# Kernel optimization log

Hardware: AMD Instinct MI355X
Metric: run time of the kernel (lower is better)

The kernel has to match this reference:

```python
import jax, jax.numpy as jnp
import numpy as np

IN_DIMS = 256
EMBED_DIMS = 512
NUM_HEADS = 8
GRID = 16  # forced: arrange2 hardcodes 256 = GRID*GRID tokens
HEAD_DIM = EMBED_DIMS // NUM_HEADS
LN_EPS = 1e-5


def setup_inputs() -> dict:
    key = jax.random.key(0)
    ks = jax.random.split(key, 12)
    B = 8
    s_in = 1.0 / np.sqrt(IN_DIMS)
    s_emb = 1.0 / np.sqrt(EMBED_DIMS)
    return {
        "x1": jax.random.normal(ks[0], (B, IN_DIMS, GRID, GRID), jnp.float32),
        "x2": jax.random.normal(ks[1], (B, IN_DIMS, GRID, GRID), jnp.float32),
        # 1x1 conv weights stored as [out, in]
        "Wq": jax.random.normal(ks[2], (EMBED_DIMS, IN_DIMS), jnp.float32) * s_in,
        "bq": jnp.zeros((EMBED_DIMS,), jnp.float32),
        "Wk": jax.random.normal(ks[3], (EMBED_DIMS, IN_DIMS), jnp.float32) * s_in,
        "bk": jnp.zeros((EMBED_DIMS,), jnp.float32),
        "Wv": jax.random.normal(ks[4], (EMBED_DIMS, IN_DIMS), jnp.float32) * s_in,
        "bv": jnp.zeros((EMBED_DIMS,), jnp.float32),
        "Wa": jax.random.normal(ks[5], (IN_DIMS, EMBED_DIMS), jnp.float32) * s_emb,
        "ba": jnp.zeros((IN_DIMS,), jnp.float32),
        "ln_g": jnp.ones((IN_DIMS,), jnp.float32),
        "ln_b": jnp.zeros((IN_DIMS,), jnp.float32),
        "Wl": jax.random.normal(ks[6], (IN_DIMS, IN_DIMS), jnp.float32) * s_in,
        "bl": jnp.zeros((IN_DIMS,), jnp.float32),
    }


def _conv1x1(x, W, b):
    # x: [b, Cin, h, w]; W: [Cout, Cin]
    return jnp.einsum('bihw,oi->bohw', x, W) + b[None, :, None, None]


def _arrange(t):
    # 'b (c head) h w -> head b (h w) c'  (c outer, head inner in channel axis)
    b = t.shape[0]
    t = t.reshape(b, HEAD_DIM, NUM_HEADS, GRID * GRID)
    return t.transpose(2, 0, 3, 1)  # [head, b, n, c]


def reference(x1, x2, Wq, bq, Wk, bk, Wv, bv, Wa, ba, ln_g, ln_b, Wl, bl):
    B, Cin, H, W = x1.shape
    N = H * W  # 256
    q = _arrange(_conv1x1(x1, Wq, bq))                     # [h, b, n, c]
    k = _arrange(_conv1x1(x2, Wk, bk))                     # [h, q, m, c]
    v = _arrange(_conv1x1(x2, Wv, bv)).reshape(NUM_HEADS, B * N, HEAD_DIM)  # [h, (b m), c]
    # cross-batch attention logits (NOTE: original never applies self.scale)
    attn = jnp.einsum('pbnc,pqmc->pbqnm', q, k)            # [h, b, q, n, m]
    attn = jax.nn.softmax(attn, axis=-1)
    # 'head b q n m -> b head n (q m)'
    attn = attn.transpose(1, 0, 3, 2, 4).reshape(B, NUM_HEADS, N, B * N)
    out = jnp.einsum('bhnm,hmc->bhnc', attn, v)            # [b, h, n, c]
    # 'b head (h w) c -> b (c head) h w'
    out = out.transpose(0, 3, 1, 2).reshape(B, EMBED_DIMS, H, W)
    a = _conv1x1(out, Wa, ba) + x1                          # residual, [b, Cin, h, w]
    # proj_out: rearrange -> LayerNorm -> Linear -> ReLU -> rearrange back
    t = a.reshape(B, Cin, N).transpose(0, 2, 1)            # [b, n, Cin]
    mu = t.mean(-1, keepdims=True)
    var = ((t - mu) ** 2).mean(-1, keepdims=True)
    t = (t - mu) * jax.lax.rsqrt(var + LN_EPS) * ln_g + ln_b
    t = jax.nn.relu(t @ Wl.T + bl)
    return t.transpose(0, 2, 1).reshape(B, Cin, H, W)
```

## Files before the change

kernel.cpp:

```cpp
#include <hip/hip_runtime.h>

typedef unsigned short u16;
typedef unsigned int   u32;
typedef __attribute__((ext_vector_type(8))) short bf16x8;
typedef __attribute__((ext_vector_type(4))) float f32x4;

#define BB   8
#define CIN  256
#define NT   256
#define EMB  512
#define NH   8

__device__ __forceinline__ float bf2f(u16 b) {
    union { u32 u; float f; } v; v.u = ((u32)b) << 16; return v.f;
}
__device__ __forceinline__ u16 f2bf(float f) {
    union { float f; u32 u; } v; v.f = f;
    u32 r = v.u + 0x7FFFu + ((v.u >> 16) & 1u);
    return (u16)(r >> 16);
}
__device__ __forceinline__ float ld(const u16* base, size_t idx, int f32) {
    return f32 ? ((const float*)base)[idx] : bf2f(base[idx]);
}

struct alignas(16) U32x4 { u32 x, y, z, w; };

#define FMA44(AP, S, A4, B4) do { \
  (AP)[0*(S)+0] += (A4).x*(B4).x; (AP)[0*(S)+1] += (A4).x*(B4).y; (AP)[0*(S)+2] += (A4).x*(B4).z; (AP)[0*(S)+3] += (A4).x*(B4).w; \
  (AP)[1*(S)+0] += (A4).y*(B4).x; (AP)[1*(S)+1] += (A4).y*(B4).y; (AP)[1*(S)+2] += (A4).y*(B4).z; (AP)[1*(S)+3] += (A4).y*(B4).w; \
  (AP)[2*(S)+0] += (A4).z*(B4).x; (AP)[2*(S)+1] += (A4).z*(B4).y; (AP)[2*(S)+2] += (A4).z*(B4).z; (AP)[2*(S)+3] += (A4).z*(B4).w; \
  (AP)[3*(S)+0] += (A4).w*(B4).x; (AP)[3*(S)+1] += (A4).w*(B4).y; (AP)[3*(S)+2] += (A4).w*(B4).z; (AP)[3*(S)+3] += (A4).w*(B4).w; \
} while (0)

__global__ void k_detect(const u16* __restrict__ x1, int* __restrict__ flag) {
    __shared__ int cnt;
    if (threadIdx.x == 0) cnt = 0;
    __syncthreads();
    int t = threadIdx.x;
    int local = 0;
    for (int j = t * 16; j < t * 16 + 16; j += 2) {
        u16 w = x1[j];
        int e = (w >> 7) & 0xFF;
        if (e >= 100 && e <= 145) local++;
    }
    atomicAdd(&cnt, local);
    __syncthreads();
    if (t == 0) *flag = (cnt >= 1200) ? 0 : 1;
}

__global__ void k_qkv(
    const u16* __restrict__ x1, const u16* __restrict__ x2,
    const u16* __restrict__ Wq, const u16* __restrict__ bq,
    const u16* __restrict__ Wk, const u16* __restrict__ bk,
    const u16* __restrict__ Wv, const u16* __restrict__ bv,
    u16* __restrict__ Qg, u16* __restrict__ Kg, u16* __restrict__ Vg,
    const int* __restrict__ flag)
{
    const int f32 = *flag;
    int id = blockIdx.x;
    int proj = id >> 8;
    int rem  = id & 255;
    int b  = rem >> 5;
    int ot = (rem >> 2) & 7;
    int nt = rem & 3;

    const u16* X    = (proj == 0) ? x1 : x2;
    const u16* W    = (proj == 0) ? Wq : (proj == 1) ? Wk : Wv;
    const u16* bias = (proj == 0) ? bq : (proj == 1) ? bk : bv;

    __shared__ float Ws[64][68];
    __shared__ float Xs[64][64];

    int t = threadIdx.x;
    int lane64 = t & 63;
    int quad   = t >> 6;
    int og = t >> 4;
    int ng = t & 15;

    float acc[16];
#pragma unroll
    for (int j = 0; j < 16; ++j) acc[j] = 0.f;

    float wreg[16], xreg[16];
#pragma unroll
    for (int p = 0; p < 16; ++p) {
        int o = quad + 4*p;
        wreg[p] = ld(W, (size_t)(ot*64 + o)*CIN + 0*64 + lane64, f32);
    }
#pragma unroll
    for (int p = 0; p < 16; ++p) {
        int i = quad + 4*p;
        xreg[p] = ld(X, ((size_t)b*CIN + 0*64 + i)*NT + nt*64 + lane64, f32);
    }

    for (int kc = 0; kc < 4; ++kc) {
        __syncthreads();
#pragma unroll
        for (int p = 0; p < 16; ++p)
            Ws[lane64][quad + 4*p] = wreg[p];
#pragma unroll
        for (int p = 0; p < 16; ++p)
            Xs[quad + 4*p][lane64] = xreg[p];
        __syncthreads();

        if (kc < 3) {
            int kn = kc + 1;
#pragma unroll
            for (int p = 0; p < 16; ++p) {
                int o = quad + 4*p;
                wreg[p] = ld(W, (size_t)(ot*64 + o)*CIN + kn*64 + lane64, f32);
            }
#pragma unroll
            for (int p = 0; p < 16; ++p) {
                int i = quad + 4*p;
                xreg[p] = ld(X, ((size_t)b*CIN + kn*64 + i)*NT + nt*64 + lane64, f32);
            }
        }

#pragma unroll 8
        for (int i = 0; i < 64; ++i) {
            float4 w4 = *(const float4*)&Ws[i][og*4];
            float4 x4 = *(const float4*)&Xs[i][ng*4];
            FMA44(acc, 4, w4, x4);
        }
    }
    __syncthreads();

#pragma unroll
    for (int jo = 0; jo < 4; ++jo) {
        int o = ot*64 + og*4 + jo;
        float bb = ld(bias, o, f32);
#pragma unroll
        for (int jn = 0; jn < 4; ++jn)
            Ws[og*4 + jo][ng*4 + jn] = acc[jo*4 + jn] + bb;
    }
    __syncthreads();

    if (proj < 2) {
        u16* OUT = (proj == 0) ? Qg : Kg;
        int hh = t >> 5;
        int nb = t & 31;
#pragma unroll
        for (int p = 0; p < 2; ++p) {
            int nn = nb + 32*p;
            u32 pk[4];
#pragma unroll
            for (int e = 0; e < 4; ++e) {
                u16 lo = f2bf(Ws[(2*e  )*8 + hh][nn]);
                u16 hi = f2bf(Ws[(2*e+1)*8 + hh][nn]);
                pk[e] = (u32)lo | ((u32)hi << 16);
            }
            U32x4 v; v.x = pk[0]; v.y = pk[1]; v.z = pk[2]; v.w = pk[3];
            *(U32x4*)&OUT[((size_t)((hh*8 + b)*256) + nt*64 + nn)*64 + ot*8] = v;
        }
    } else {
        int rr = t >> 2;
        int hh = rr & 7, cl = rr >> 3;
        int nq = t & 3;
        u32 pk[8];
#pragma unroll
        for (int e = 0; e < 8; ++e) {
            u16 lo = f2bf(Ws[cl*8 + hh][nq*16 + 2*e  ]);
            u16 hi = f2bf(Ws[cl*8 + hh][nq*16 + 2*e+1]);
            pk[e] = (u32)lo | ((u32)hi << 16);
        }
        size_t base = ((size_t)((hh*8 + b)*64) + ot*8 + cl)*256 + nt*64 + nq*16;
        U32x4 v0; v0.x = pk[0]; v0.y = pk[1]; v0.z = pk[2]; v0.w = pk[3];
        U32x4 v1; v1.x = pk[4]; v1.y = pk[5]; v1.z = pk[6]; v1.w = pk[7];
        *(U32x4*)&Vg[base]     = v0;
        *(U32x4*)&Vg[base + 8] = v1;
    }
}

__global__ __launch_bounds__(256) void k_attn(
    const u16* __restrict__ Qg, const u16* __restrict__ Kg,
    const u16* __restrict__ Vg, float* __restrict__ Oph)
{
    int bid = blockIdx.x;
    int h   = bid >> 5;
    int b   = (bid >> 2) & 7;
    int ntq = bid & 3;

    int t = threadIdx.x;
    int l = t & 63, w = t >> 6;
    int quad = l >> 4, col = l & 15;

    __shared__ __align__(16) u16 S[16896];

    int q = ntq*64 + w*16 + col;
    const size_t qrow = ((size_t)(h*8 + b)*256 + q)*64;
    bf16x8 qf0 = *(const bf16x8*)&Qg[qrow +  0 + quad*8];
    bf16x8 qf1 = *(const bf16x8*)&Qg[qrow + 32 + quad*8];

    const int lswz2 = l ^ (((l >> 4) & 1) << 1);
    const int lswz4 = l ^ (((l >> 4) & 1) << 2);

    f32x4 Oacc[4];
#pragma unroll
    for (int ct = 0; ct < 4; ++ct) { Oacc[ct][0]=0.f; Oacc[ct][1]=0.f; Oacc[ct][2]=0.f; Oacc[ct][3]=0.f; }

    for (int kb = 0; kb < 8; ++kb) {
        __syncthreads();
        const size_t kbase = (size_t)(h*8 + kb) * 256 * 64;
#pragma unroll
        for (int i = 0; i < 8; ++i) {
            int g = i*256 + t;
            int key = g >> 3, cc = g & 7;
            int tt = key >> 4, klo = key & 15, kc = cc >> 2, qs = cc & 3;
            int pos = qs*16 + (klo ^ ((qs & 1) << 1) ^ (kc << 2));
            U32x4 v = *(const U32x4*)&Kg[kbase + (size_t)key*64 + cc*8];
            *(U32x4*)&S[(size_t)(((tt*2 + kc)*64) + pos)*8] = v;
        }
        __syncthreads();

        f32x4 Sfr[16];
#pragma unroll
        for (int tt = 0; tt < 16; ++tt) { Sfr[tt][0]=0.f; Sfr[tt][1]=0.f; Sfr[tt][2]=0.f; Sfr[tt][3]=0.f; }
#pragma unroll
        for (int tt = 0; tt < 16; ++tt) {
            bf16x8 k0 = *(const bf16x8*)&S[(size_t)((tt*2 + 0)*64 + lswz2)*8];
            bf16x8 k1 = *(const bf16x8*)&S[(size_t)((tt*2 + 1)*64 + (lswz2 ^ 4))*8];
            Sfr[tt] = __builtin_amdgcn_mfma_f32_16x16x32_bf16(qf0, k0, Sfr[tt], 0, 0, 0);
            Sfr[tt] = __builtin_amdgcn_mfma_f32_16x16x32_bf16(qf1, k1, Sfr[tt], 0, 0, 0);
        }

        float inv[4];
#pragma unroll
        for (int r = 0; r < 4; ++r) {
            float m = Sfr[0][r];
#pragma unroll
            for (int tt = 1; tt < 16; ++tt) m = fmaxf(m, Sfr[tt][r]);
#pragma unroll
            for (int off = 1; off < 16; off <<= 1) m = fmaxf(m, __shfl_xor(m, off));
            float s = 0.f;
#pragma unroll
            for (int tt = 0; tt < 16; ++tt) {
                float e = __expf(Sfr[tt][r] - m);
                Sfr[tt][r] = e; s += e;
            }
#pragma unroll
            for (int off = 1; off < 16; off <<= 1) s += __shfl_xor(s, off);
            inv[r] = 1.f / s;
        }
        __syncthreads();

#pragma unroll
        for (int tt = 0; tt < 16; ++tt)
#pragma unroll
            for (int e = 0; e < 2; ++e) {
                u32 pk = (u32)f2bf(Sfr[tt][2*e]   * inv[2*e]) |
                        ((u32)f2bf(Sfr[tt][2*e+1] * inv[2*e+1]) << 16);
                *(u32*)&S[(tt*16 + col)*66 + w*16 + quad*4 + 2*e] = pk;
            }

        bf16x8 pf[8];
#pragma unroll
        for (int ch = 0; ch < 8; ++ch)
#pragma unroll
            for (int j = 0; j < 8; ++j)
                pf[ch][j] = (short)S[(ch*32 + quad*8 + j)*66 + w*16 + col];
        __syncthreads();

        const size_t vbase = (size_t)(h*8 + kb) * 64 * 256;
#pragma unroll
        for (int i = 0; i < 8; ++i) {
            int g = i*256 + t;
            int cg = g >> 5, k16 = g & 31;
            int ct = cg >> 4, clo = cg & 15, ch = k16 >> 2, qs = k16 & 3;
            int pos = (qs*16 + clo) ^ ch ^ ((qs & 1) << 2);
            U32x4 v = *(const U32x4*)&Vg[vbase + (size_t)cg*256 + k16*8];
            *(U32x4*)&S[(size_t)(((ch*4 + ct)*64) + pos)*8] = v;
        }
        __syncthreads();

#pragma unroll
        for (int ch = 0; ch < 8; ++ch)
#pragma unroll
            for (int ct = 0; ct < 4; ++ct) {
                bf16x8 vb = *(const bf16x8*)&S[(size_t)(((ch*4 + ct)*64) + (lswz4 ^ ch))*8];
                Oacc[ct] = __builtin_amdgcn_mfma_f32_16x16x32_bf16(pf[ch], vb, Oacc[ct], 0, 0, 0);
            }
    }

    const size_t obase = (size_t)(h*8 + b) * 256 * 64;
    int n0 = ntq*64 + w*16 + quad*4;
#pragma unroll
    for (int ct = 0; ct < 4; ++ct)
#pragma unroll
        for (int r = 0; r < 4; ++r)
            Oph[obase + (size_t)(n0 + r)*64 + ct*16 + col] = Oacc[ct][r];
}

__global__ void k_proj_res(
    const float* __restrict__ Oph, const u16* __restrict__ Wa,
    const u16* __restrict__ ba, const u16* __restrict__ x1,
    float* __restrict__ Ap, const int* __restrict__ flag)
{
    const int f32 = *flag;
    int id = blockIdx.x;
    int tt = id >> 2;
    int it = id & 3;
    int tok0 = tt * 32;
    int b  = tok0 >> 8;
    int n0 = tok0 & 255;

    __shared__ float Was[64][68];
    __shared__ float Os[64][36];

    int t = threadIdx.x;
    int lane64 = t & 63, quad = t >> 6;
    int ig = t & 15;
    int tg = t >> 4;

    int tk = t & 31;
    int hh = t >> 5;

    float wreg[16];
    float oreg[8];

    {
#pragma unroll
        for (int p = 0; p < 16; ++p) {
            int i = quad + 4*p;
            wreg[p] = ld(Wa, (size_t)(it*64 + i)*EMB + 0*64 + lane64, f32);
        }
        const float* src = &Oph[(((size_t)(hh*8 + b))*256 + n0 + tk)*64 + 0*8];
        float4 v0 = *(const float4*)&src[0];
        float4 v1 = *(const float4*)&src[4];
        oreg[0]=v0.x; oreg[1]=v0.y; oreg[2]=v0.z; oreg[3]=v0.w;
        oreg[4]=v1.x; oreg[5]=v1.y; oreg[6]=v1.z; oreg[7]=v1.w;
    }

    float acc[8];
#pragma unroll
    for (int j = 0; j < 8; ++j) acc[j] = 0.f;

    for (int kc = 0; kc < 8; ++kc) {
        __syncthreads();
#pragma unroll
        for (int p = 0; p < 16; ++p)
            Was[lane64][quad + 4*p] = wreg[p];
#pragma unroll
        for (int e = 0; e < 8; ++e)
            Os[e*8 + hh][tk] = oreg[e];
        __syncthreads();

        if (kc < 7) {
            int kn = kc + 1;
#pragma unroll
            for (int p = 0; p < 16; ++p) {
                int i = quad + 4*p;
                wreg[p] = ld(Wa, (size_t)(it*64 + i)*EMB + kn*64 + lane64, f32);
            }
            const float* src = &Oph[(((size_t)(hh*8 + b))*256 + n0 + tk)*64 + kn*8];
            float4 v0 = *(const float4*)&src[0];
            float4 v1 = *(const float4*)&src[4];
            oreg[0]=v0.x; oreg[1]=v0.y; oreg[2]=v0.z; oreg[3]=v0.w;
            oreg[4]=v1.x; oreg[5]=v1.y; oreg[6]=v1.z; oreg[7]=v1.w;
        }

#pragma unroll 8
        for (int o = 0; o < 64; ++o) {
            float4 w4 = *(const float4*)&Was[o][ig*4];
            float2 t2 = *(const float2*)&Os[o][tg*2];
            acc[0] += w4.x*t2.x; acc[1] += w4.y*t2.x;
            acc[2] += w4.z*t2.x; acc[3] += w4.w*t2.x;
            acc[4] += w4.x*t2.y; acc[5] += w4.y*t2.y;
            acc[6] += w4.z*t2.y; acc[7] += w4.w*t2.y;
        }
    }

    int i0 = it*64 + ig*4;
    float ba0 = ld(ba, i0+0, f32), ba1 = ld(ba, i0+1, f32);
    float ba2 = ld(ba, i0+2, f32), ba3 = ld(ba, i0+3, f32);
#pragma unroll
    for (int jt = 0; jt < 2; ++jt) {
        int token = tok0 + tg*2 + jt;
        int n = n0 + tg*2 + jt;
        float4 v;
        v.x = acc[jt*4+0] + ba0 + ld(x1, ((size_t)b*CIN + i0+0)*NT + n, f32);
        v.y = acc[jt*4+1] + ba1 + ld(x1, ((size_t)b*CIN + i0+1)*NT + n, f32);
        v.z = acc[jt*4+2] + ba2 + ld(x1, ((size_t)b*CIN + i0+2)*NT + n, f32);
        v.w = acc[jt*4+3] + ba3 + ld(x1, ((size_t)b*CIN + i0+3)*NT + n, f32);
        *(float4*)&Ap[(size_t)token*CIN + i0] = v;
    }
}

__global__ void k_ln_out(
    const float* __restrict__ Ap, const u16* __restrict__ ln_g,
    const u16* __restrict__ ln_b, const u16* __restrict__ Wl,
    const u16* __restrict__ bl, u16* __restrict__ out,
    const int* __restrict__ flag)
{
    const int f32 = *flag;
    int tok0 = blockIdx.x * 8;
    int b  = tok0 >> 8;
    int n0 = tok0 & 255;

    __shared__ float At[8][260];

    int t = threadIdx.x;
#pragma unroll
    for (int k = 0; k < 8; ++k)
        At[k][t] = Ap[((size_t)tok0 + k)*CIN + t];
    __syncthreads();

    {
        int kk = t >> 5, lme = t & 31;
        float s = 0.f, s2 = 0.f;
#pragma unroll
        for (int ii = 0; ii < 8; ++ii) { float v = At[kk][lme + 32*ii]; s += v; s2 += v*v; }
#pragma unroll
        for (int off = 1; off < 32; off <<= 1) { s += __shfl_xor(s, off); s2 += __shfl_xor(s2, off); }
        float mu   = s  * (1.f/256.f);
        float var  = s2 * (1.f/256.f) - mu*mu;
        float rstd = rsqrtf(var + 1e-5f);
#pragma unroll
        for (int ii = 0; ii < 8; ++ii) {
            int i = lme + 32*ii;
            float v = At[kk][i];
            At[kk][i] = (v - mu) * rstd * ld(ln_g, i, f32) + ld(ln_b, i, f32);
        }
    }
    __syncthreads();

    int j = t;
    float acc[8];
#pragma unroll
    for (int k = 0; k < 8; ++k) acc[k] = 0.f;

    if (f32) {
        const float* wrow = (const float*)Wl + (size_t)j*CIN;
#pragma unroll 2
        for (int i4 = 0; i4 < 64; ++i4) {
            float4 w4 = *(const float4*)&wrow[4*i4];
#pragma unroll
            for (int k = 0; k < 8; ++k) {
                float4 a = *(const float4*)&At[k][4*i4];
                acc[k] += w4.x*a.x + w4.y*a.y + w4.z*a.z + w4.w*a.w;
            }
        }
    } else {
        const u32* wrow = (const u32*)(Wl + (size_t)j*CIN);
#pragma unroll 2
        for (int i4 = 0; i4 < 64; ++i4) {
            u32 w01 = wrow[2*i4+0], w23 = wrow[2*i4+1];
            float c0 = bf2f((u16)(w01 & 0xFFFFu)), c1 = bf2f((u16)(w01 >> 16));
            float c2 = bf2f((u16)(w23 & 0xFFFFu)), c3 = bf2f((u16)(w23 >> 16));
#pragma unroll
            for (int k = 0; k < 8; ++k) {
                float4 a = *(const float4*)&At[k][4*i4];
                acc[k] += c0*a.x + c1*a.y + c2*a.z + c3*a.w;
            }
        }
    }

    float blv = ld(bl, j, f32);
    size_t obase = ((size_t)b*CIN + j)*NT + n0;
    if (f32) {
        float* o32 = (float*)out;
#pragma unroll
        for (int k = 0; k < 8; ++k)
            o32[obase + k] = fmaxf(acc[k] + blv, 0.f);
    } else {
        u32 pk[4];
#pragma unroll
        for (int k = 0; k < 4; ++k) {
            float f0 = fmaxf(acc[2*k+0] + blv, 0.f);
            float f1 = fmaxf(acc[2*k+1] + blv, 0.f);
            pk[k] = (u32)f2bf(f0) | ((u32)f2bf(f1) << 16);
        }
        U32x4 a0; a0.x = pk[0]; a0.y = pk[1]; a0.z = pk[2]; a0.w = pk[3];
        *(U32x4*)(out + obase) = a0;
    }
}

extern "C" void kernel_launch(void* const* d_in, const int* in_sizes, int n_in,
                              void* d_out, int out_size, void* d_ws, size_t ws_size,
                              hipStream_t stream)
{
    const u16* x1   = (const u16*)d_in[0];
    const u16* x2   = (const u16*)d_in[1];
    const u16* Wq   = (const u16*)d_in[2];
    const u16* bq   = (const u16*)d_in[3];
    const u16* Wk   = (const u16*)d_in[4];
    const u16* bk   = (const u16*)d_in[5];
    const u16* Wv   = (const u16*)d_in[6];
    const u16* bv   = (const u16*)d_in[7];
    const u16* Wa   = (const u16*)d_in[8];
    const u16* ba   = (const u16*)d_in[9];
    const u16* ln_g = (const u16*)d_in[10];
    const u16* ln_b = (const u16*)d_in[11];
    const u16* Wl   = (const u16*)d_in[12];
    const u16* bl   = (const u16*)d_in[13];
    u16* out = (u16*)d_out;

    int* flag = (int*)d_ws;
    u16* Qg = (u16*)d_ws + 32;
    u16* Kg = Qg + (size_t)BB*EMB*NT;
    u16* Vg = Kg + (size_t)BB*EMB*NT;
    float* Oph = (float*)(Vg + (size_t)BB*EMB*NT);
    float* Ap  = Oph + (size_t)BB*EMB*NT;

    k_detect  <<<1,   256, 0, stream>>>(x1, flag);
    k_qkv     <<<768, 256, 0, stream>>>(x1, x2, Wq, bq, Wk, bk, Wv, bv, Qg, Kg, Vg, flag);
    k_attn    <<<256, 256, 0, stream>>>(Qg, Kg, Vg, Oph);
    k_proj_res<<<256, 256, 0, stream>>>(Oph, Wa, ba, x1, Ap, flag);
    k_ln_out  <<<256, 256, 0, stream>>>(Ap, ln_g, ln_b, Wl, bl, out, flag);
}
```

Measured before the change: 206.0 us.

## Split attention key batches across two blocks and build P in registers

The attention kernel now launches twice as many blocks. Each block handles half of the key batches and accumulates its partial output into Oph with atomicAdd, after a memset zeroes Oph. This is valid because softmax is normalized independently per key batch. The QK MFMA operands are swapped so each lane holds logits for one query row, which lets the probability fragments be packed with cvt_pk_bf16 and permlane swaps instead of a round trip through shared memory. The change adds atomic traffic and a memset in exchange for more parallelism and fewer LDS accesses and barriers.

```diff
diff --git a/kernel.cpp b/kernel.cpp
--- a/kernel.cpp
+++ b/kernel.cpp
@@ -177,7 +177,8 @@
     const u16* __restrict__ Vg, float* __restrict__ Oph)
 {
     int bid = blockIdx.x;
-    int h   = bid >> 5;
+    int h   = bid >> 6;
+    int kbg = (bid >> 5) & 1;
     int b   = (bid >> 2) & 7;
     int ntq = bid & 3;
 
@@ -185,7 +186,7 @@
     int l = t & 63, w = t >> 6;
     int quad = l >> 4, col = l & 15;
 
-    __shared__ __align__(16) u16 S[16896];
+    __shared__ __align__(16) u16 S[16384];
 
     int q = ntq*64 + w*16 + col;
     const size_t qrow = ((size_t)(h*8 + b)*256 + q)*64;
@@ -199,7 +200,8 @@
 #pragma unroll
     for (int ct = 0; ct < 4; ++ct) { Oacc[ct][0]=0.f; Oacc[ct][1]=0.f; Oacc[ct][2]=0.f; Oacc[ct][3]=0.f; }
 
-    for (int kb = 0; kb < 8; ++kb) {
+    for (int kb2 = 0; kb2 < 4; ++kb2) {
+        int kb = kbg*4 + kb2;
         __syncthreads();
         const size_t kbase = (size_t)(h*8 + kb) * 256 * 64;
 #pragma unroll
@@ -220,45 +222,52 @@
         for (int tt = 0; tt < 16; ++tt) {
             bf16x8 k0 = *(const bf16x8*)&S[(size_t)((tt*2 + 0)*64 + lswz2)*8];
             bf16x8 k1 = *(const bf16x8*)&S[(size_t)((tt*2 + 1)*64 + (lswz2 ^ 4))*8];
-            Sfr[tt] = __builtin_amdgcn_mfma_f32_16x16x32_bf16(qf0, k0, Sfr[tt], 0, 0, 0);
-            Sfr[tt] = __builtin_amdgcn_mfma_f32_16x16x32_bf16(qf1, k1, Sfr[tt], 0, 0, 0);
-        }
-
-        float inv[4];
-#pragma unroll
-        for (int r = 0; r < 4; ++r) {
-            float m = Sfr[0][r];
-#pragma unroll
-            for (int tt = 1; tt < 16; ++tt) m = fmaxf(m, Sfr[tt][r]);
-#pragma unroll
-            for (int off = 1; off < 16; off <<= 1) m = fmaxf(m, __shfl_xor(m, off));
+            Sfr[tt] = __builtin_amdgcn_mfma_f32_16x16x32_bf16(k0, qf0, Sfr[tt], 0, 0, 0);
+            Sfr[tt] = __builtin_amdgcn_mfma_f32_16x16x32_bf16(k1, qf1, Sfr[tt], 0, 0, 0);
+        }
+
+        float inv;
+        {
+            float m = Sfr[0][0];
+#pragma unroll
+            for (int tt = 0; tt < 16; ++tt)
+#pragma unroll
+                for (int r = 0; r < 4; ++r) m = fmaxf(m, Sfr[tt][r]);
+            m = fmaxf(m, __shfl_xor(m, 16));
+            m = fmaxf(m, __shfl_xor(m, 32));
             float s = 0.f;
 #pragma unroll
-            for (int tt = 0; tt < 16; ++tt) {
-                float e = __expf(Sfr[tt][r] - m);
-                Sfr[tt][r] = e; s += e;
-            }
-#pragma unroll
-            for (int off = 1; off < 16; off <<= 1) s += __shfl_xor(s, off);
-            inv[r] = 1.f / s;
-        }
-        __syncthreads();
-
-#pragma unroll
-        for (int tt = 0; tt < 16; ++tt)
-#pragma unroll
-            for (int e = 0; e < 2; ++e) {
-                u32 pk = (u32)f2bf(Sfr[tt][2*e]   * inv[2*e]) |
-                        ((u32)f2bf(Sfr[tt][2*e+1] * inv[2*e+1]) << 16);
-                *(u32*)&S[(tt*16 + col)*66 + w*16 + quad*4 + 2*e] = pk;
-            }
+            for (int tt = 0; tt < 16; ++tt)
+#pragma unroll
+                for (int r = 0; r < 4; ++r) {
+                    float e = __expf(Sfr[tt][r] - m);
+                    Sfr[tt][r] = e; s += e;
+                }
+            s += __shfl_xor(s, 16);
+            s += __shfl_xor(s, 32);
+            inv = 1.f / s;
+        }
 
         bf16x8 pf[8];
 #pragma unroll
-        for (int ch = 0; ch < 8; ++ch)
-#pragma unroll
-            for (int j = 0; j < 8; ++j)
-                pf[ch][j] = (short)S[(ch*32 + quad*8 + j)*66 + w*16 + col];
+        for (int ch = 0; ch < 8; ++ch) {
+            float a0 = Sfr[2*ch  ][0]*inv, a1 = Sfr[2*ch  ][1]*inv;
+            float a2 = Sfr[2*ch  ][2]*inv, a3 = Sfr[2*ch  ][3]*inv;
+            float b0 = Sfr[2*ch+1][0]*inv, b1 = Sfr[2*ch+1][1]*inv;
+            float b2 = Sfr[2*ch+1][2]*inv, b3 = Sfr[2*ch+1][3]*inv;
+            u32 u0, u1, v0, v1;
+            asm("v_cvt_pk_bf16_f32 %0, %1, %2" : "=v"(u0) : "v"(a0), "v"(a1));
+            asm("v_cvt_pk_bf16_f32 %0, %1, %2" : "=v"(u1) : "v"(a2), "v"(a3));
+            asm("v_cvt_pk_bf16_f32 %0, %1, %2" : "=v"(v0) : "v"(b0), "v"(b1));
+            asm("v_cvt_pk_bf16_f32 %0, %1, %2" : "=v"(v1) : "v"(b2), "v"(b3));
+            asm("v_permlane32_swap_b32 %0, %1" : "+v"(u0), "+v"(v0));
+            asm("v_permlane16_swap_b32 %0, %1" : "+v"(u0), "+v"(v0));
+            asm("v_permlane32_swap_b32 %0, %1" : "+v"(u1), "+v"(v1));
+            asm("v_permlane16_swap_b32 %0, %1" : "+v"(u1), "+v"(v1));
+            union { u32 wd[4]; bf16x8 hB; } pu;
+            pu.wd[0] = u0; pu.wd[1] = u1; pu.wd[2] = v0; pu.wd[3] = v1;
+            pf[ch] = pu.hB;
+        }
         __syncthreads();
 
         const size_t vbase = (size_t)(h*8 + kb) * 64 * 256;
@@ -288,7 +297,7 @@
     for (int ct = 0; ct < 4; ++ct)
 #pragma unroll
         for (int r = 0; r < 4; ++r)
-            Oph[obase + (size_t)(n0 + r)*64 + ct*16 + col] = Oacc[ct][r];
+            atomicAdd(&Oph[obase + (size_t)(n0 + r)*64 + ct*16 + col], Oacc[ct][r]);
 }
 
 __global__ void k_proj_res(
@@ -502,9 +511,11 @@
     float* Oph = (float*)(Vg + (size_t)BB*EMB*NT);
     float* Ap  = Oph + (size_t)BB*EMB*NT;
 
+    hipMemsetAsync(Oph, 0, (size_t)BB*EMB*NT*sizeof(float), stream);
+
     k_detect  <<<1,   256, 0, stream>>>(x1, flag);
     k_qkv     <<<768, 256, 0, stream>>>(x1, x2, Wq, bq, Wk, bk, Wv, bv, Qg, Kg, Vg, flag);
-    k_attn    <<<256, 256, 0, stream>>>(Qg, Kg, Vg, Oph);
+    k_attn    <<<512, 256, 0, stream>>>(Qg, Kg, Vg, Oph);
     k_proj_res<<<256, 256, 0, stream>>>(Oph, Wa, ba, x1, Ap, flag);
     k_ln_out  <<<256, 256, 0, stream>>>(Ap, ln_g, ln_b, Wl, bl, out, flag);
 }
```

Measured after the change: 187.3 us. 1.1x faster.
